# Kernel tuning notes

Measured on AMD Instinct MI355X. Metric: run time of the kernel, lower is better.

Reference implementation:

```python
import jax, jax.numpy as jnp
import numpy as np

PERIOD = 24
NUM_ITERATIONS = 2


def _window_size():
    w = max(3, PERIOD // 2)  # 12
    if w % 2 == 0:
        w += 1  # 13
    return w


def moving_average(s, w):
    # s: [N, L]; replicate-pad by w//2 on each side, then width-w mean conv ('VALID')
    pad = w // 2
    sp = jnp.pad(s, ((0, 0), (pad, pad)), mode='edge')[:, None, :]  # [N,1,L+2*pad]
    k = jnp.ones((1, 1, w), s.dtype) / w
    y = jax.lax.conv_general_dilated(sp, k, window_strides=(1,), padding='VALID',
                                     dimension_numbers=('NCH', 'OIH', 'NCH'))
    return y[:, 0, :]  # [N, L]


def extract_seasonal(d):
    # d: [N, L] with L a multiple of PERIOD. Strided indices i, i+P, ... correspond
    # to reshape [N, C, P] with fixed last axis; median over cycles, broadcast back.
    N, L = d.shape
    C = L // PERIOD
    sub = d.reshape(N, C, PERIOD)
    med = jnp.median(sub, axis=1)  # [N, P] (C=121 is odd -> matches torch.median)
    return jnp.broadcast_to(med[:, None, :], (N, C, PERIOD)).reshape(N, L)


def setup_inputs() -> dict:
    key = jax.random.key(0)
    x = jax.random.normal(key, (64, 2904, 207), dtype=jnp.float32)
    return {"x": x}


def reference(x):
    # x: [B, L, F] -> process all features at once as [B*F, L]
    B, L, F = x.shape
    s = jnp.transpose(x, (0, 2, 1)).reshape(B * F, L)
    w = _window_size()
    trend = moving_average(s, w)
    for _ in range(NUM_ITERATIONS):
        seasonal = extract_seasonal(s - trend)
        trend = moving_average(s - seasonal, w)
    residual = s - trend - seasonal

    def unflatten(a):
        return jnp.transpose(a.reshape(B, F, L), (0, 2, 1))  # [B, L, F]

    return unflatten(trend), unflatten(seasonal), unflatten(residual)
```

## Files before the change

kernel.cpp:

```cpp
#include <hip/hip_runtime.h>

#define LROW    2904
#define PERIOD  24
#define CYC     121
#define NF      207
#define NB      64
#define NROWS   13248
#define NSLOT   61
#define NT      256
#define LTILE   24
#define NLT     121
#define K2GRID  (NB * NLT)
#define K2CHUNK (K2GRID / 8)
#define R13     (1.f / 13.f)
#define KROW    (PERIOD * 64)
#define KBAND   ((size_t)NSLOT * KROW)

typedef unsigned short us2 __attribute__((ext_vector_type(2)));

__device__ __forceinline__ int clampi(int i) {
    return i < 0 ? 0 : (i >= LROW ? LROW - 1 : i);
}
__device__ __forceinline__ unsigned quantk(float d) {
    int ki = (int)fmaf(d, 4096.f, 32768.f);
    ki = ki < 0 ? 0 : (ki > 65535 ? 65535 : ki);
    return (unsigned)ki;
}
__device__ __forceinline__ float dqmid(unsigned k) {
    return ((float)(int)k - 32767.5f) * (1.f / 4096.f);
}

__device__ __forceinline__ unsigned sel60(const unsigned (&K)[NSLOT]) {
    unsigned T = 0;
    const us2 one2 = __builtin_bit_cast(us2, 0x00010001u);
    for (int bit = 15; bit >= 0; --bit) {
        unsigned Tp = T | (1u << bit);
        unsigned tm32 = (Tp - 1u) | ((Tp - 1u) << 16);
        us2 tm2 = __builtin_bit_cast(us2, tm32);
        us2 acc = __builtin_bit_cast(us2, 0u);
        #pragma unroll
        for (int s = 0; s < NSLOT; ++s) {
            us2 kv = __builtin_bit_cast(us2, K[s]);
            us2 dd = __builtin_elementwise_sub_sat(kv, tm2);
            us2 mm = __builtin_elementwise_min(dd, one2);
            acc = acc + mm;
        }
        unsigned a = __builtin_bit_cast(unsigned, acc);
        int cnt = (int)(a & 0xFFFFu) + (int)(a >> 16);
        if (cnt >= 62) T = Tp;
    }
    return T;
}

__global__ __launch_bounds__(256) void k_keys(const float* __restrict__ x,
                                              unsigned* __restrict__ keys) {
    const int b   = blockIdx.x;
    const int ft  = blockIdx.y;
    const int wid = threadIdx.x >> 6;
    const int seg = wid * 8 + blockIdx.z;
    const int fl  = threadIdx.x & 63;
    const int f   = ft * 64 + fl;
    const int fe  = f < NF ? f : NF - 1;
    if (seg > 30) return;
    const int c0 = seg * 4;
    const float* xb = x + (size_t)b * (LROW * NF) + fe;
    unsigned* kb = keys + (size_t)(b * 4 + ft) * KBAND + fl;

    float r[13];
    const int l0 = c0 * PERIOD;
    #pragma unroll
    for (int i = 0; i < 13; ++i) {
        int l = l0 - 7 + i; if (l < 0) l = 0;
        r[i] = xb[(size_t)l * NF];
    }
    unsigned pend[PERIOD];
    if (seg < 30) {
        #pragma unroll
        for (int cc = 0; cc < 4; ++cc) {
            const int c = c0 + cc;
            const int lb = c * PERIOD;
            const int slot = c >> 1;
            float sum = ((r[0] + r[1]) + (r[2] + r[3]))
                      + ((r[4] + r[5]) + (r[6] + r[7]))
                      + ((r[8] + r[9]) + (r[10] + r[11])) + r[12];
            #pragma unroll
            for (int s = 0; s < PERIOD; ++s) {
                float xn = xb[(size_t)(lb + s + 6) * NF];
                sum += xn - r[0];
                unsigned k = quantk(r[7] - sum * R13);
                if ((cc & 1) == 0) {
                    pend[s] = k;
                } else {
                    kb[(size_t)(slot * PERIOD + s) * 64] = pend[s] | (k << 16);
                }
                #pragma unroll
                for (int i = 0; i < 12; ++i) r[i] = r[i + 1];
                r[12] = xn;
            }
        }
    } else {
        const int lb = 120 * PERIOD;
        float sum = ((r[0] + r[1]) + (r[2] + r[3]))
                  + ((r[4] + r[5]) + (r[6] + r[7]))
                  + ((r[8] + r[9]) + (r[10] + r[11])) + r[12];
        #pragma unroll
        for (int s = 0; s < PERIOD; ++s) {
            int ll = lb + s + 6; if (ll > LROW - 1) ll = LROW - 1;
            float xn = xb[(size_t)ll * NF];
            sum += xn - r[0];
            unsigned k = quantk(r[7] - sum * R13);
            kb[(size_t)(60 * PERIOD + s) * 64] = k | 0xFFFF0000u;
            #pragma unroll
            for (int i = 0; i < 12; ++i) r[i] = r[i + 1];
            r[12] = xn;
        }
    }
}

__global__ __launch_bounds__(256) void k_med0(const unsigned* __restrict__ keys,
                                              unsigned short* __restrict__ med0key) {
    const int d  = blockIdx.x;
    const int bp = (d & 7) * 192 + (d >> 3);
    const int b = bp / PERIOD, p = bp - b * PERIOD;
    const int ft = threadIdx.x >> 6, fl = threadIdx.x & 63;
    const int f = ft * 64 + fl;
    unsigned K[NSLOT];
    const unsigned* kp = keys + (size_t)(b * 4 + ft) * KBAND + p * 64 + fl;
    #pragma unroll
    for (int s = 0; s < NSLOT; ++s) K[s] = kp[(size_t)s * KROW];
    unsigned T = sel60(K);
    if (f < NF) med0key[(size_t)bp * NF + f] = (unsigned short)T;
}

__global__ __launch_bounds__(256) void k_edge(const unsigned* __restrict__ keys,
                                              const unsigned short* __restrict__ med0key,
                                              float* __restrict__ medBedge) {
    const int d  = blockIdx.x;
    const int bj = (d & 7) * 48 + (d >> 3);
    const int b = bj / 6, j = bj - 6 * b;
    const int ft = threadIdx.x >> 6, fl = threadIdx.x & 63;
    const int f = ft * 64 + fl;
    const int fe = f < NF ? f : NF - 1;

    float m0[PERIOD];
    #pragma unroll
    for (int p = 0; p < PERIOD; ++p)
        m0[p] = dqmid(med0key[(size_t)(b * PERIOD + p) * NF + fe]);

    float wA = 0.f, wB = 0.f, weA = 0.f, weB = 0.f;
    #pragma unroll
    for (int jj = 0; jj < 6; ++jj) if (jj == j) {
        #pragma unroll
        for (int t = 0; t < 13; ++t) {
            wA += m0[(jj + 18 + t) % 24];
            wB += m0[(jj + 12 + t) % 24];
        }
        #pragma unroll
        for (int t = -6; t <= 6; ++t) {
            int aa = jj + t;       if (aa < 0)  aa = 0;
            int bb = 18 + jj + t;  if (bb > 23) bb = 23;
            weA += m0[aa];
            weB += m0[bb];
        }
    }

    unsigned K[NSLOT];
    {
        const unsigned* kp = keys + (size_t)(b * 4 + ft) * KBAND + j * 64 + fl;
        #pragma unroll
        for (int s = 0; s < NSLOT; ++s) K[s] = kp[(size_t)s * KROW];
        unsigned kn = quantk(dqmid(K[0] & 0xFFFFu) + (weA - wA) * R13);
        K[0] = (K[0] & 0xFFFF0000u) | kn;
        unsigned T = sel60(K);
        if (f < NF) medBedge[(size_t)(b * 12 + j) * NF + f] = dqmid(T) + wA * R13;
    }
    {
        const unsigned* kp = keys + (size_t)(b * 4 + ft) * KBAND + (18 + j) * 64 + fl;
        #pragma unroll
        for (int s = 0; s < NSLOT; ++s) K[s] = kp[(size_t)s * KROW];
        unsigned kn = quantk(dqmid(K[60] & 0xFFFFu) + (weB - wB) * R13);
        K[60] = (K[60] & 0xFFFF0000u) | kn;
        unsigned T = sel60(K);
        if (f < NF) medBedge[(size_t)(b * 12 + 6 + j) * NF + f] = dqmid(T) + wB * R13;
    }
}

__global__ __launch_bounds__(64) void k_final(const unsigned short* __restrict__ med0key,
                                              const float* __restrict__ medBedge,
                                              float* __restrict__ wsTab) {
    const int blk = blockIdx.x;
    const int b = blk >> 2, ft = blk & 3;
    const int lane = threadIdx.x;
    const int f = ft * 64 + lane;
    const int fe = f < NF ? f : NF - 1;

    float m0[PERIOD], mB[PERIOD];
    #pragma unroll
    for (int p = 0; p < PERIOD; ++p)
        m0[p] = dqmid(med0key[(size_t)(b * PERIOD + p) * NF + fe]);
    float W0[PERIOD];
    {
        float s = 0.f;
        #pragma unroll
        for (int t = 0; t < 13; ++t) s += m0[t];
        W0[0] = s;
        #pragma unroll
        for (int q = 1; q < PERIOD; ++q)
            W0[q] = W0[q - 1] + m0[(q + 12) % 24] - m0[q - 1];
    }
    #pragma unroll
    for (int e = 0; e < 12; ++e) {
        int p = (e < 6) ? e : e + 12;
        mB[p] = medBedge[(size_t)(b * 12 + e) * NF + fe];
    }
    #pragma unroll
    for (int p = 6; p < 18; ++p) mB[p] = m0[p] + W0[p - 6] * R13;
    float W1[PERIOD];
    {
        float s = 0.f;
        #pragma unroll
        for (int t = 0; t < 13; ++t) s += mB[t];
        W1[0] = s;
        #pragma unroll
        for (int q = 1; q < PERIOD; ++q)
            W1[q] = W1[q - 1] + mB[(q + 12) % 24] - mB[q - 1];
    }
    if (f < NF) {
        #pragma unroll
        for (int p = 0; p < PERIOD; ++p) {
            wsTab[((size_t)b * 48 + p) * NF + f]      = mB[p];
            wsTab[((size_t)b * 48 + 24 + p) * NF + f] = W1[p];
        }
    }
}

__global__ __launch_bounds__(NT, 5) void stl_outputs(const float* __restrict__ x,
                                                     const float* __restrict__ ws,
                                                     float* __restrict__ out) {
    __shared__ float T[(LTILE + 12) * NF];

    const int d   = blockIdx.x;
    const int blk = (d & 7) * K2CHUNK + (d >> 3);
    const int b  = blk / NLT;
    const int kk = blk - b * NLT;
    const int l0 = kk * LTILE;
    const int t  = threadIdx.x;
    const float* xb = x + (size_t)b * (LROW * NF);

    if (kk != 0 && kk != NLT - 1) {
        const float2* s2 = (const float2*)(xb + (size_t)(l0 - 6) * NF);
        float2* t2 = (float2*)T;
        for (int i = t; i < (LTILE + 12) * NF / 2; i += NT) t2[i] = s2[i];
    } else {
        for (int i = t; i < (LTILE + 12) * NF; i += NT) {
            int lr = i / NF;
            int ff = i - lr * NF;
            T[i] = xb[(size_t)clampi(l0 - 6 + lr) * NF + ff];
        }
    }
    __syncthreads();

    if (t < NF) {
        float lm[PERIOD], wt[PERIOD];
        const float* wrow = ws + (size_t)b * 48 * NF + t;
        #pragma unroll
        for (int i = 0; i < PERIOD; ++i) lm[i] = wrow[i * NF];
        #pragma unroll
        for (int i = 0; i < PERIOD; ++i) wt[i] = wrow[(PERIOD + i) * NF];

        float s13 = 0.f;
        #pragma unroll
        for (int r = 0; r < 13; ++r) s13 += T[r * NF + t];

        const bool edgeLo = (kk == 0), edgeHi = (kk == NLT - 1);
        const size_t S = (size_t)NROWS * LROW;
        const size_t obase = (size_t)b * (LROW * NF) + (size_t)l0 * NF + (size_t)t;

        #pragma unroll
        for (int j = 0; j < LTILE; ++j) {
            float W = wt[(j + 18) % 24];
            if (edgeLo && j < 6) {
                float w = 0.f;
                #pragma unroll
                for (int jj = -6; jj <= 6; ++jj) { int m = j + jj; if (m < 0) m = 0; w += lm[m]; }
                W = w;
            }
            if (edgeHi && j >= 18) {
                float w = 0.f;
                #pragma unroll
                for (int jj = -6; jj <= 6; ++jj) { int m = j + jj; if (m > 23) m = 23; w += lm[m]; }
                W = w;
            }
            float tr = (s13 - W) * R13;
            float se = lm[j];
            float re = T[(j + 6) * NF + t] - tr - se;
            size_t o = obase + (size_t)(j * NF);
            __builtin_nontemporal_store(tr, &out[o]);
            __builtin_nontemporal_store(se, &out[S + o]);
            __builtin_nontemporal_store(re, &out[2 * S + o]);
            if (j < LTILE - 1)
                s13 += T[(j + 13) * NF + t] - T[j * NF + t];
        }
    }
}

extern "C" void kernel_launch(void* const* d_in, const int* in_sizes, int n_in,
                              void* d_out, int out_size, void* d_ws, size_t ws_size,
                              hipStream_t stream) {
    const float* x = (const float*)d_in[0];
    float* out = (float*)d_out;
    float* wsf = (float*)d_ws;
    (void)in_sizes; (void)n_in; (void)out_size; (void)ws_size;

    float*    wsTab    = wsf;
    unsigned* keys     = (unsigned*)(wsf + 635904);
    float*    medBedge = wsf + 635904 + 23986176;
    unsigned short* med0key = (unsigned short*)(wsf + 635904 + 23986176 + 158976);

    hipLaunchKernelGGL(k_keys,   dim3(NB, 4, 8), dim3(256), 0, stream, x, keys);
    hipLaunchKernelGGL(k_med0,   dim3(NB * PERIOD), dim3(256), 0, stream, keys, med0key);
    hipLaunchKernelGGL(k_edge,   dim3(NB * 6), dim3(256), 0, stream, keys, med0key, medBedge);
    hipLaunchKernelGGL(k_final,  dim3(NB * 4), dim3(64), 0, stream, med0key, medBedge, wsTab);
    hipLaunchKernelGGL(stl_outputs, dim3(K2GRID), dim3(NT), 0, stream, x, wsTab, out);
}
```

Baseline: 345.3 us.

## Stage input tiles in LDS for key generation and flatten key layout per feature

The key-generation kernel now launches one block per (batch, cycle pair) that cooperatively copies a contiguous 62-row slab of the input into shared memory with float2 loads, then each thread computes its feature's moving-average keys from LDS. Before, each thread issued strided global loads with feature tiling. The key buffer layout changes from per-64-feature bands to a per-(batch,phase) stride padded to 256 features, so the median and edge kernels use one thread per feature. This is meant to improve coalescing and cut redundant global reads, at the cost of about 50KB of LDS per block, which limits occupancy.

Result: slower. 357.1 us (+3.4%).

```diff
diff --git a/kernel.cpp b/kernel.cpp
--- a/kernel.cpp
+++ b/kernel.cpp
@@ -7,14 +7,14 @@
 #define NB      64
 #define NROWS   13248
 #define NSLOT   61
+#define KPAD    256
+#define KSTRIDE (NSLOT * KPAD)
 #define NT      256
 #define LTILE   24
 #define NLT     121
 #define K2GRID  (NB * NLT)
 #define K2CHUNK (K2GRID / 8)
 #define R13     (1.f / 13.f)
-#define KROW    (PERIOD * 64)
-#define KBAND   ((size_t)NSLOT * KROW)
 
 typedef unsigned short us2 __attribute__((ext_vector_type(2)));
 
@@ -54,62 +54,53 @@
 
 __global__ __launch_bounds__(256) void k_keys(const float* __restrict__ x,
                                               unsigned* __restrict__ keys) {
-    const int b   = blockIdx.x;
-    const int ft  = blockIdx.y;
-    const int wid = threadIdx.x >> 6;
-    const int seg = wid * 8 + blockIdx.z;
-    const int fl  = threadIdx.x & 63;
-    const int f   = ft * 64 + fl;
-    const int fe  = f < NF ? f : NF - 1;
-    if (seg > 30) return;
-    const int c0 = seg * 4;
-    const float* xb = x + (size_t)b * (LROW * NF) + fe;
-    unsigned* kb = keys + (size_t)(b * 4 + ft) * KBAND + fl;
+    __shared__ float T[62 * NF];
+    const int b  = blockIdx.x;
+    const int cp = blockIdx.y;
+    const int fl = threadIdx.x;
+    const int fe = fl < NF ? fl : NF - 1;
+    const int l0 = cp * 48;
+    const float* xb = x + (size_t)b * (LROW * NF);
+    unsigned* kb = keys + ((size_t)b * PERIOD * NSLOT + cp) * KPAD + fl;
+
+    if (cp != 0 && cp != 60) {
+        const float2* s2 = (const float2*)(xb + (size_t)(l0 - 8) * NF);
+        float2* t2 = (float2*)T;
+        for (int i = fl; i < 62 * NF / 2; i += NT) t2[i] = s2[i];
+    } else {
+        for (int i = fl; i < 62 * NF; i += NT) {
+            int lr = i / NF, ff = i - lr * NF;
+            T[i] = xb[(size_t)clampi(l0 - 8 + lr) * NF + ff];
+        }
+    }
+    __syncthreads();
 
     float r[13];
-    const int l0 = c0 * PERIOD;
-    #pragma unroll
-    for (int i = 0; i < 13; ++i) {
-        int l = l0 - 7 + i; if (l < 0) l = 0;
-        r[i] = xb[(size_t)l * NF];
-    }
-    unsigned pend[PERIOD];
-    if (seg < 30) {
-        #pragma unroll
-        for (int cc = 0; cc < 4; ++cc) {
-            const int c = c0 + cc;
-            const int lb = c * PERIOD;
-            const int slot = c >> 1;
-            float sum = ((r[0] + r[1]) + (r[2] + r[3]))
-                      + ((r[4] + r[5]) + (r[6] + r[7]))
-                      + ((r[8] + r[9]) + (r[10] + r[11])) + r[12];
-            #pragma unroll
-            for (int s = 0; s < PERIOD; ++s) {
-                float xn = xb[(size_t)(lb + s + 6) * NF];
-                sum += xn - r[0];
-                unsigned k = quantk(r[7] - sum * R13);
-                if ((cc & 1) == 0) {
-                    pend[s] = k;
-                } else {
-                    kb[(size_t)(slot * PERIOD + s) * 64] = pend[s] | (k << 16);
-                }
-                #pragma unroll
-                for (int i = 0; i < 12; ++i) r[i] = r[i + 1];
-                r[12] = xn;
-            }
-        }
-    } else {
-        const int lb = 120 * PERIOD;
-        float sum = ((r[0] + r[1]) + (r[2] + r[3]))
-                  + ((r[4] + r[5]) + (r[6] + r[7]))
-                  + ((r[8] + r[9]) + (r[10] + r[11])) + r[12];
-        #pragma unroll
-        for (int s = 0; s < PERIOD; ++s) {
-            int ll = lb + s + 6; if (ll > LROW - 1) ll = LROW - 1;
-            float xn = xb[(size_t)ll * NF];
+    #pragma unroll
+    for (int i = 0; i < 13; ++i) r[i] = T[(i + 1) * NF + fe];
+    float sum = ((r[0] + r[1]) + (r[2] + r[3])) + ((r[4] + r[5]) + (r[6] + r[7]))
+              + ((r[8] + r[9]) + (r[10] + r[11])) + r[12];
+
+    if (cp < 60) {
+        unsigned pend[PERIOD];
+        #pragma unroll
+        for (int j = 0; j < 48; ++j) {
+            float xn = T[(j + 14) * NF + fe];
             sum += xn - r[0];
             unsigned k = quantk(r[7] - sum * R13);
-            kb[(size_t)(60 * PERIOD + s) * 64] = k | 0xFFFF0000u;
+            if (j < 24) pend[j] = k;
+            else kb[(size_t)(j - 24) * KSTRIDE] = pend[j - 24] | (k << 16);
+            #pragma unroll
+            for (int i = 0; i < 12; ++i) r[i] = r[i + 1];
+            r[12] = xn;
+        }
+    } else {
+        #pragma unroll
+        for (int j = 0; j < 24; ++j) {
+            float xn = T[(j + 14) * NF + fe];
+            sum += xn - r[0];
+            unsigned k = quantk(r[7] - sum * R13);
+            kb[(size_t)j * KSTRIDE] = k | 0xFFFF0000u;
             #pragma unroll
             for (int i = 0; i < 12; ++i) r[i] = r[i + 1];
             r[12] = xn;
@@ -121,15 +112,13 @@
                                               unsigned short* __restrict__ med0key) {
     const int d  = blockIdx.x;
     const int bp = (d & 7) * 192 + (d >> 3);
-    const int b = bp / PERIOD, p = bp - b * PERIOD;
-    const int ft = threadIdx.x >> 6, fl = threadIdx.x & 63;
-    const int f = ft * 64 + fl;
+    const int fl = threadIdx.x;
     unsigned K[NSLOT];
-    const unsigned* kp = keys + (size_t)(b * 4 + ft) * KBAND + p * 64 + fl;
-    #pragma unroll
-    for (int s = 0; s < NSLOT; ++s) K[s] = kp[(size_t)s * KROW];
+    const unsigned* kp = keys + (size_t)bp * KSTRIDE + fl;
+    #pragma unroll
+    for (int s = 0; s < NSLOT; ++s) K[s] = kp[(size_t)s * KPAD];
     unsigned T = sel60(K);
-    if (f < NF) med0key[(size_t)bp * NF + f] = (unsigned short)T;
+    if (fl < NF) med0key[(size_t)bp * NF + fl] = (unsigned short)T;
 }
 
 __global__ __launch_bounds__(256) void k_edge(const unsigned* __restrict__ keys,
@@ -138,9 +127,8 @@
     const int d  = blockIdx.x;
     const int bj = (d & 7) * 48 + (d >> 3);
     const int b = bj / 6, j = bj - 6 * b;
-    const int ft = threadIdx.x >> 6, fl = threadIdx.x & 63;
-    const int f = ft * 64 + fl;
-    const int fe = f < NF ? f : NF - 1;
+    const int fl = threadIdx.x;
+    const int fe = fl < NF ? fl : NF - 1;
 
     float m0[PERIOD];
     #pragma unroll
@@ -166,22 +154,22 @@
 
     unsigned K[NSLOT];
     {
-        const unsigned* kp = keys + (size_t)(b * 4 + ft) * KBAND + j * 64 + fl;
-        #pragma unroll
-        for (int s = 0; s < NSLOT; ++s) K[s] = kp[(size_t)s * KROW];
+        const unsigned* kp = keys + (size_t)(b * PERIOD + j) * KSTRIDE + fl;
+        #pragma unroll
+        for (int s = 0; s < NSLOT; ++s) K[s] = kp[(size_t)s * KPAD];
         unsigned kn = quantk(dqmid(K[0] & 0xFFFFu) + (weA - wA) * R13);
         K[0] = (K[0] & 0xFFFF0000u) | kn;
         unsigned T = sel60(K);
-        if (f < NF) medBedge[(size_t)(b * 12 + j) * NF + f] = dqmid(T) + wA * R13;
+        if (fl < NF) medBedge[(size_t)(b * 12 + j) * NF + fl] = dqmid(T) + wA * R13;
     }
     {
-        const unsigned* kp = keys + (size_t)(b * 4 + ft) * KBAND + (18 + j) * 64 + fl;
-        #pragma unroll
-        for (int s = 0; s < NSLOT; ++s) K[s] = kp[(size_t)s * KROW];
+        const unsigned* kp = keys + (size_t)(b * PERIOD + 18 + j) * KSTRIDE + fl;
+        #pragma unroll
+        for (int s = 0; s < NSLOT; ++s) K[s] = kp[(size_t)s * KPAD];
         unsigned kn = quantk(dqmid(K[60] & 0xFFFFu) + (weB - wB) * R13);
         K[60] = (K[60] & 0xFFFF0000u) | kn;
         unsigned T = sel60(K);
-        if (f < NF) medBedge[(size_t)(b * 12 + 6 + j) * NF + f] = dqmid(T) + wB * R13;
+        if (fl < NF) medBedge[(size_t)(b * 12 + 6 + j) * NF + fl] = dqmid(T) + wB * R13;
     }
 }
 
@@ -317,9 +305,9 @@
     float*    medBedge = wsf + 635904 + 23986176;
     unsigned short* med0key = (unsigned short*)(wsf + 635904 + 23986176 + 158976);
 
-    hipLaunchKernelGGL(k_keys,   dim3(NB, 4, 8), dim3(256), 0, stream, x, keys);
-    hipLaunchKernelGGL(k_med0,   dim3(NB * PERIOD), dim3(256), 0, stream, keys, med0key);
-    hipLaunchKernelGGL(k_edge,   dim3(NB * 6), dim3(256), 0, stream, keys, med0key, medBedge);
+    hipLaunchKernelGGL(k_keys,   dim3(NB, NSLOT), dim3(NT), 0, stream, x, keys);
+    hipLaunchKernelGGL(k_med0,   dim3(NB * PERIOD), dim3(NT), 0, stream, keys, med0key);
+    hipLaunchKernelGGL(k_edge,   dim3(NB * 6), dim3(NT), 0, stream, keys, med0key, medBedge);
     hipLaunchKernelGGL(k_final,  dim3(NB * 4), dim3(64), 0, stream, med0key, medBedge, wsTab);
     hipLaunchKernelGGL(stl_outputs, dim3(K2GRID), dim3(NT), 0, stream, x, wsTab, out);
 }
```
